# Kernel tuning notes

Measured on AMD Instinct MI355X. Metric: run time of the kernel, lower is better.

Reference implementation:

```python
import jax, jax.numpy as jnp
import numpy as np

DIM = 96
DIM_OUT = 192
HEADS = 2
Q_STRIDE = 4
WINDOW_SIZE = 16  # flattened mask-unit size AFTER q pooling
HEAD_DIM = DIM_OUT // HEADS


def setup_inputs() -> dict:
    key = jax.random.key(0)
    k1, k2, k3, k4, k5 = jax.random.split(key, 5)
    B, N = 64, 3136  # 56x56 tokens, 49 windows of 64 tokens
    x = jax.random.normal(k1, (B, N, DIM), dtype=jnp.float32)
    # nn.Linear params (PyTorch layout: [out, in])
    s_qkv = 1.0 / np.sqrt(DIM)
    w_qkv = jax.random.uniform(k2, (3 * DIM_OUT, DIM), jnp.float32, -s_qkv, s_qkv)
    b_qkv = jax.random.uniform(k3, (3 * DIM_OUT,), jnp.float32, -s_qkv, s_qkv)
    s_proj = 1.0 / np.sqrt(DIM_OUT)
    w_proj = jax.random.uniform(k4, (DIM_OUT, DIM_OUT), jnp.float32, -s_proj, s_proj)
    b_proj = jax.random.uniform(k5, (DIM_OUT,), jnp.float32, -s_proj, s_proj)
    return {"x": x, "w_qkv": w_qkv, "b_qkv": b_qkv, "w_proj": w_proj, "b_proj": b_proj}


def reference(x, w_qkv, b_qkv, w_proj, b_proj):
    B, N, _ = x.shape
    num_windows = N // (Q_STRIDE * WINDOW_SIZE)
    tokens_per_win = Q_STRIDE * WINDOW_SIZE  # 64
    # QKV projection; token axis splits as (tokens_per_win, num_windows)
    qkv = (x @ w_qkv.T + b_qkv).reshape(B, tokens_per_win, num_windows, 3, HEADS, HEAD_DIM)
    qkv = jnp.transpose(qkv, (3, 0, 4, 2, 1, 5))  # [3, B, H, W, T, D]
    q, k, v = qkv[0], qkv[1], qkv[2]
    # q pooling via strided amax over q_stride
    q = q.reshape(B, HEADS, num_windows, Q_STRIDE, WINDOW_SIZE, HEAD_DIM).max(axis=3)
    scale = HEAD_DIM ** (-0.5)
    attn = jax.nn.softmax(jnp.einsum('bhwqd,bhwkd->bhwqk', q * scale, k), axis=-1)
    o = jnp.einsum('bhwqk,bhwkd->bhwqd', attn, v)  # [B, H, W, WINDOW_SIZE, D]
    # transpose(1,3) then flatten -> [B, WINDOW_SIZE*num_windows, dim_out]
    o = jnp.transpose(o, (0, 3, 2, 1, 4)).reshape(B, -1, DIM_OUT)
    return o @ w_proj.T + b_proj
```

## Files before the change

### kernel.cpp

```cpp
#include <hip/hip_runtime.h>


#define NW 49
#define NTOK 3136
#define DIM 96
#define DOUT 192

#define WSQ 0
#define WSBQ 55296
#define WSP 55872
#define WSBP 92736
#define WSTOT 92928

typedef __bf16 bf16x8 __attribute__((ext_vector_type(8)));
typedef float f32x4 __attribute__((ext_vector_type(4)));
typedef unsigned short u16x8 __attribute__((ext_vector_type(8)));
typedef unsigned short u16x4 __attribute__((ext_vector_type(4)));

__device__ __forceinline__ unsigned short f2bf(float f) {
    return __builtin_bit_cast(unsigned short, (__bf16)f);
}
__device__ __forceinline__ float bf2f(unsigned short h) {
    unsigned int u = ((unsigned int)h) << 16;
    return __builtin_bit_cast(float, u);
}

__device__ __forceinline__ bool sniff_fp32(const unsigned short* x16) {
    int sane = 0;
    #pragma unroll
    for (int i = 0; i < 32; ++i) {
        unsigned e = ((unsigned)x16[2 * i] >> 7) & 0xFFu;
        sane += (e >= 100u && e <= 141u) ? 1 : 0;
    }
    return sane < 24;
}

__device__ __forceinline__ bf16x8 ldb(const unsigned short* p) {
    return __builtin_bit_cast(bf16x8, *(const u16x8*)p);
}

__global__ __launch_bounds__(256)
void conv_weights(const void* __restrict__ x,
                  const void* __restrict__ w_qkv, const void* __restrict__ b_qkv,
                  const void* __restrict__ w_proj, const void* __restrict__ b_proj,
                  unsigned short* __restrict__ ws)
{
    const bool f32m = sniff_fp32((const unsigned short*)x);
    int t = blockIdx.x * 256 + threadIdx.x;
    if (t >= WSTOT / 8) return;
    int off = t * 8;
    const void* src;
    int rel;
    if (off < WSBQ)      { src = w_qkv;  rel = off; }
    else if (off < WSP)  { src = b_qkv;  rel = off - WSBQ; }
    else if (off < WSBP) { src = w_proj; rel = off - WSP; }
    else                 { src = b_proj; rel = off - WSBP; }
    u16x8 v;
    if (f32m) {
        const float* p = (const float*)src + rel;
        f32x4 a = *(const f32x4*)p;
        f32x4 bb = *(const f32x4*)(p + 4);
        v[0] = f2bf(a[0]);  v[1] = f2bf(a[1]);  v[2] = f2bf(a[2]);  v[3] = f2bf(a[3]);
        v[4] = f2bf(bb[0]); v[5] = f2bf(bb[1]); v[6] = f2bf(bb[2]); v[7] = f2bf(bb[3]);
    } else {
        v = *(const u16x8*)((const unsigned short*)src + rel);
    }
    *(u16x8*)(ws + off) = v;
}

__global__ __launch_bounds__(256, 2)
void mua_main(const void* __restrict__ x,
              const unsigned short* __restrict__ ws,
              void* __restrict__ out)
{
    const int bid = blockIdx.x;
    const int b   = bid / NW;
    const int wi  = bid - b * NW;
    const int tid  = threadIdx.x;
    const int wave = tid >> 6;
    const int lane = tid & 63;
    const int quad = lane >> 4;
    const int l16  = lane & 15;

    __shared__ __attribute__((aligned(16))) unsigned short lds[19456];
    unsigned short* x_s  = lds;
    unsigned short* k_s  = lds;
    unsigned short* v_s  = lds;
    unsigned short* qp_s = lds + 13824;
    unsigned short* o_s  = lds + 13824;
    unsigned short* p_s  = lds + 17152;

    bf16x8 wq[3][3];
    float  biasq[6];
    #pragma unroll
    for (int nt = 0; nt < 3; ++nt) {
        const int c = (nt * 4 + wave) * 16 + l16;
        #pragma unroll
        for (int ks = 0; ks < 3; ++ks)
            wq[nt][ks] = ldb(ws + WSQ + c * 96 + ks * 32 + quad * 8);
    }
    #pragma unroll
    for (int nt = 0; nt < 6; ++nt)
        biasq[nt] = bf2f(ws[WSBQ + (nt * 4 + wave) * 16 + l16]);

    const bool f32m = sniff_fp32((const unsigned short*)x);

    {
        const size_t xoff = ((size_t)b * NTOK + wi) * DIM;
        if (f32m) {
            #pragma unroll
            for (int i = 0; i < 3; ++i) {
                int chunk = tid + i * 256;
                int row = chunk / 12;
                int c16 = chunk - row * 12;
                const float* p = (const float*)x + xoff + (size_t)row * (NW * DIM) + c16 * 8;
                f32x4 a = *(const f32x4*)p;
                f32x4 bb = *(const f32x4*)(p + 4);
                u16x8 r;
                r[0] = f2bf(a[0]);  r[1] = f2bf(a[1]);  r[2] = f2bf(a[2]);  r[3] = f2bf(a[3]);
                r[4] = f2bf(bb[0]); r[5] = f2bf(bb[1]); r[6] = f2bf(bb[2]); r[7] = f2bf(bb[3]);
                *(u16x8*)&x_s[row * 104 + c16 * 8] = r;
            }
        } else {
            #pragma unroll
            for (int i = 0; i < 3; ++i) {
                int chunk = tid + i * 256;
                int row = chunk / 12;
                int c16 = chunk - row * 12;
                const unsigned short* p = (const unsigned short*)x + xoff + (size_t)row * (NW * DIM) + c16 * 8;
                *(u16x8*)&x_s[row * 104 + c16 * 8] = *(const u16x8*)p;
            }
        }
    }
    __syncthreads();

    bf16x8 afr[4][3];
    #pragma unroll
    for (int mt = 0; mt < 4; ++mt)
        #pragma unroll
        for (int ks = 0; ks < 3; ++ks)
            afr[mt][ks] = ldb(&x_s[(mt * 16 + l16) * 104 + ks * 32 + quad * 8]);
    __syncthreads();

    #pragma unroll
    for (int nt = 0; nt < 6; ++nt) {
        const int slot = nt % 3;
        f32x4 acc[4];
        #pragma unroll
        for (int mt = 0; mt < 4; ++mt) {
            acc[mt] = (f32x4){0.f, 0.f, 0.f, 0.f};
            #pragma unroll
            for (int ks = 0; ks < 3; ++ks)
                acc[mt] = __builtin_amdgcn_mfma_f32_16x16x32_bf16(afr[mt][ks], wq[slot][ks], acc[mt], 0, 0, 0);
        }
        if (nt < 3) {
            const int c2 = ((nt + 3) * 4 + wave) * 16 + l16;
            #pragma unroll
            for (int ks = 0; ks < 3; ++ks)
                wq[slot][ks] = ldb(ws + WSQ + c2 * 96 + ks * 32 + quad * 8);
        }
        const int tt = nt * 4 + wave;
        const float bias = biasq[nt];
        if (nt < 3) {
            const int hd = tt / 6;
            const int d  = (tt % 6) * 16 + l16;
            #pragma unroll
            for (int r = 0; r < 4; ++r) {
                float m = fmaxf(fmaxf(acc[0][r], acc[1][r]), fmaxf(acc[2][r], acc[3][r])) + bias;
                qp_s[(hd * 16 + quad * 4 + r) * 104 + d] = f2bf(m);
            }
        } else {
            const int tk = tt - 12;
            const int hd = tk / 6;
            const int d  = (tk % 6) * 16 + l16;
            #pragma unroll
            for (int mt = 0; mt < 4; ++mt)
                #pragma unroll
                for (int r = 0; r < 4; ++r)
                    k_s[hd * 6656 + (mt * 16 + quad * 4 + r) * 104 + d] = f2bf(acc[mt][r] + bias);
        }
    }
    __syncthreads();

    const int h   = wave >> 1;
    const int sub = wave & 1;
    bf16x8 qa[3];
    #pragma unroll
    for (int ks = 0; ks < 3; ++ks)
        qa[ks] = ldb(&qp_s[(h * 16 + l16) * 104 + ks * 32 + quad * 8]);
    f32x4 s[4];
    #pragma unroll
    for (int nt = 0; nt < 4; ++nt) {
        s[nt] = (f32x4){0.f, 0.f, 0.f, 0.f};
        #pragma unroll
        for (int ks = 0; ks < 3; ++ks) {
            bf16x8 kb = ldb(&k_s[h * 6656 + (nt * 16 + l16) * 104 + ks * 32 + quad * 8]);
            s[nt] = __builtin_amdgcn_mfma_f32_16x16x32_bf16(qa[ks], kb, s[nt], 0, 0, 0);
        }
    }
    float rinv[4];
    const float cexp = 0.10206207261596576f * 1.4426950408889634f;
    #pragma unroll
    for (int r = 0; r < 4; ++r) {
        float m = fmaxf(fmaxf(s[0][r], s[1][r]), fmaxf(s[2][r], s[3][r]));
        m = fmaxf(m, __shfl_xor(m, 1));
        m = fmaxf(m, __shfl_xor(m, 2));
        m = fmaxf(m, __shfl_xor(m, 4));
        m = fmaxf(m, __shfl_xor(m, 8));
        float sum = 0.f;
        #pragma unroll
        for (int nt = 0; nt < 4; ++nt) {
            s[nt][r] = exp2f((s[nt][r] - m) * cexp);
            sum += s[nt][r];
        }
        sum += __shfl_xor(sum, 1);
        sum += __shfl_xor(sum, 2);
        sum += __shfl_xor(sum, 4);
        sum += __shfl_xor(sum, 8);
        rinv[r] = 1.0f / sum;
    }
    if (sub == 0) {
        #pragma unroll
        for (int nt = 0; nt < 4; ++nt)
            #pragma unroll
            for (int r = 0; r < 4; ++r)
                p_s[h * 1152 + (quad * 4 + r) * 72 + nt * 16 + l16] = f2bf(s[nt][r]);
    }

    bf16x8 wv[2][3];
    float  biasv[3];
    #pragma unroll
    for (int i = 0; i < 2; ++i) {
        const int c = 384 + (i * 4 + wave) * 16 + l16;
        #pragma unroll
        for (int ks = 0; ks < 3; ++ks)
            wv[i][ks] = ldb(ws + WSQ + c * 96 + ks * 32 + quad * 8);
    }
    #pragma unroll
    for (int i = 0; i < 3; ++i)
        biasv[i] = bf2f(ws[WSBQ + 384 + (i * 4 + wave) * 16 + l16]);
    __syncthreads();

    #pragma unroll
    for (int i = 0; i < 3; ++i) {
        const int slot = i & 1;
        f32x4 acc[4];
        #pragma unroll
        for (int mt = 0; mt < 4; ++mt) {
            acc[mt] = (f32x4){0.f, 0.f, 0.f, 0.f};
            #pragma unroll
            for (int ks = 0; ks < 3; ++ks)
                acc[mt] = __builtin_amdgcn_mfma_f32_16x16x32_bf16(afr[mt][ks], wv[slot][ks], acc[mt], 0, 0, 0);
        }
        if (i == 0) {
            const int c2 = 384 + (2 * 4 + wave) * 16 + l16;
            #pragma unroll
            for (int ks = 0; ks < 3; ++ks)
                wv[0][ks] = ldb(ws + WSQ + c2 * 96 + ks * 32 + quad * 8);
        }
        const int tv = i * 4 + wave;
        const int hd = tv / 6;
        const int d  = (tv % 6) * 16 + l16;
        const float bias = biasv[i];
        #pragma unroll
        for (int mt = 0; mt < 4; ++mt) {
            u16x4 pk;
            #pragma unroll
            for (int r = 0; r < 4; ++r) pk[r] = f2bf(acc[mt][r] + bias);
            *(u16x4*)&v_s[hd * 6912 + d * 72 + mt * 16 + quad * 4] = pk;
        }
    }

    const int cbase = wave * 48;
    bf16x8 wpr[3][6];
    float  biasp[3];
    #pragma unroll
    for (int i = 0; i < 3; ++i) {
        const int c = cbase + i * 16 + l16;
        #pragma unroll
        for (int ks = 0; ks < 6; ++ks)
            wpr[i][ks] = ldb(ws + WSP + c * 192 + ks * 32 + quad * 8);
        biasp[i] = bf2f(ws[WSBP + c]);
    }
    __syncthreads();

    bf16x8 pa[2];
    #pragma unroll
    for (int ks = 0; ks < 2; ++ks)
        pa[ks] = ldb(&p_s[h * 1152 + l16 * 72 + ks * 32 + quad * 8]);
    #pragma unroll
    for (int i = 0; i < 3; ++i) {
        const int n0 = (sub * 3 + i) * 16;
        f32x4 oacc = (f32x4){0.f, 0.f, 0.f, 0.f};
        #pragma unroll
        for (int ks = 0; ks < 2; ++ks) {
            bf16x8 vb = ldb(&v_s[h * 6912 + (n0 + l16) * 72 + ks * 32 + quad * 8]);
            oacc = __builtin_amdgcn_mfma_f32_16x16x32_bf16(pa[ks], vb, oacc, 0, 0, 0);
        }
        #pragma unroll
        for (int r = 0; r < 4; ++r)
            o_s[(quad * 4 + r) * 200 + h * 96 + n0 + l16] = f2bf(oacc[r] * rinv[r]);
    }
    __syncthreads();

    bf16x8 oa[6];
    #pragma unroll
    for (int ks = 0; ks < 6; ++ks)
        oa[ks] = ldb(&o_s[l16 * 200 + ks * 32 + quad * 8]);
    #pragma unroll
    for (int i = 0; i < 3; ++i) {
        const int c = cbase + i * 16 + l16;
        f32x4 acc = (f32x4){0.f, 0.f, 0.f, 0.f};
        #pragma unroll
        for (int ks = 0; ks < 6; ++ks)
            acc = __builtin_amdgcn_mfma_f32_16x16x32_bf16(oa[ks], wpr[i][ks], acc, 0, 0, 0);
        const float bias = biasp[i];
        #pragma unroll
        for (int r = 0; r < 4; ++r) {
            const int m = quad * 4 + r;
            const size_t idx = ((size_t)(b * 784 + m * NW + wi)) * DOUT + c;
            if (f32m) ((float*)out)[idx] = acc[r] + bias;
            else      ((unsigned short*)out)[idx] = f2bf(acc[r] + bias);
        }
    }
}

extern "C" void kernel_launch(void* const* d_in, const int* in_sizes, int n_in,
                              void* d_out, int out_size, void* d_ws, size_t ws_size,
                              hipStream_t stream) {
    const void* x      = d_in[0];
    const void* w_qkv  = d_in[1];
    const void* b_qkv  = d_in[2];
    const void* w_proj = d_in[3];
    const void* b_proj = d_in[4];
    unsigned short* ws = (unsigned short*)d_ws;

    dim3 gridc((WSTOT / 8 + 255) / 256), blockc(256);
    hipLaunchKernelGGL(conv_weights, gridc, blockc, 0, stream,
                       x, w_qkv, b_qkv, w_proj, b_proj, ws);

    dim3 grid(64 * NW), block(256);
    hipLaunchKernelGGL(mua_main, grid, block, 0, stream, x, ws, d_out);
}
```

Baseline: 176.3 us.

## Compute transposed scores, keep softmax probs in registers, swizzle K/V LDS layouts

The score MFMA now computes S^T (K as the A operand) so each lane holds a full key column. The softmax reduction then uses only cross-quad shuffles. The probabilities are repacked into the PV A-operand with register shuffles instead of going through a p_s LDS buffer. K and V tiles move from padded strides to XOR-swizzled unpadded layouts, which shrinks LDS from 19456 to 15616 shorts and aims to avoid bank conflicts. This removes one LDS round trip and cuts LDS footprint, at the cost of many extra __shfl operations and more complex indexing.

```diff
diff --git a/kernel.cpp b/kernel.cpp
--- a/kernel.cpp
+++ b/kernel.cpp
@@ -16,6 +16,7 @@
 typedef float f32x4 __attribute__((ext_vector_type(4)));
 typedef unsigned short u16x8 __attribute__((ext_vector_type(8)));
 typedef unsigned short u16x4 __attribute__((ext_vector_type(4)));
+typedef unsigned int   u32x4 __attribute__((ext_vector_type(4)));
 
 __device__ __forceinline__ unsigned short f2bf(float f) {
     return __builtin_bit_cast(unsigned short, (__bf16)f);
@@ -82,13 +83,12 @@
     const int quad = lane >> 4;
     const int l16  = lane & 15;
 
-    __shared__ __attribute__((aligned(16))) unsigned short lds[19456];
+    __shared__ __attribute__((aligned(16))) unsigned short lds[15616];
     unsigned short* x_s  = lds;
     unsigned short* k_s  = lds;
     unsigned short* v_s  = lds;
-    unsigned short* qp_s = lds + 13824;
-    unsigned short* o_s  = lds + 13824;
-    unsigned short* p_s  = lds + 17152;
+    unsigned short* qp_s = lds + 12288;
+    unsigned short* o_s  = lds + 12288;
 
     bf16x8 wq[3][3];
     float  biasq[6];
@@ -172,12 +172,14 @@
         } else {
             const int tk = tt - 12;
             const int hd = tk / 6;
-            const int d  = (tk % 6) * 16 + l16;
+            const int dbh  = ((tk % 6) * 16) / 8 + (l16 >> 3);
+            const int dlow = l16 & 7;
             #pragma unroll
             for (int mt = 0; mt < 4; ++mt)
                 #pragma unroll
                 for (int r = 0; r < 4; ++r)
-                    k_s[hd * 6656 + (mt * 16 + quad * 4 + r) * 104 + d] = f2bf(acc[mt][r] + bias);
+                    k_s[hd * 6144 + (mt * 16 + quad * 4 + r) * 96 + ((dbh ^ r) << 3) + dlow]
+                        = f2bf(acc[mt][r] + bias);
         }
     }
     __syncthreads();
@@ -188,43 +190,72 @@
     #pragma unroll
     for (int ks = 0; ks < 3; ++ks)
         qa[ks] = ldb(&qp_s[(h * 16 + l16) * 104 + ks * 32 + quad * 8]);
-    f32x4 s[4];
-    #pragma unroll
-    for (int nt = 0; nt < 4; ++nt) {
-        s[nt] = (f32x4){0.f, 0.f, 0.f, 0.f};
-        #pragma unroll
-        for (int ks = 0; ks < 3; ++ks) {
-            bf16x8 kb = ldb(&k_s[h * 6656 + (nt * 16 + l16) * 104 + ks * 32 + quad * 8]);
-            s[nt] = __builtin_amdgcn_mfma_f32_16x16x32_bf16(qa[ks], kb, s[nt], 0, 0, 0);
-        }
-    }
-    float rinv[4];
+    f32x4 st[4];
+    #pragma unroll
+    for (int mt = 0; mt < 4; ++mt) st[mt] = (f32x4){0.f, 0.f, 0.f, 0.f};
+    #pragma unroll
+    for (int ks = 0; ks < 3; ++ks)
+        #pragma unroll
+        for (int mt = 0; mt < 4; ++mt) {
+            bf16x8 kb = ldb(&k_s[h * 6144 + (mt * 16 + l16) * 96 + (((ks * 4 + quad) ^ (l16 & 3)) << 3)]);
+            st[mt] = __builtin_amdgcn_mfma_f32_16x16x32_bf16(kb, qa[ks], st[mt], 0, 0, 0);
+        }
     const float cexp = 0.10206207261596576f * 1.4426950408889634f;
-    #pragma unroll
-    for (int r = 0; r < 4; ++r) {
-        float m = fmaxf(fmaxf(s[0][r], s[1][r]), fmaxf(s[2][r], s[3][r]));
-        m = fmaxf(m, __shfl_xor(m, 1));
-        m = fmaxf(m, __shfl_xor(m, 2));
-        m = fmaxf(m, __shfl_xor(m, 4));
-        m = fmaxf(m, __shfl_xor(m, 8));
-        float sum = 0.f;
-        #pragma unroll
-        for (int nt = 0; nt < 4; ++nt) {
-            s[nt][r] = exp2f((s[nt][r] - m) * cexp);
-            sum += s[nt][r];
-        }
-        sum += __shfl_xor(sum, 1);
-        sum += __shfl_xor(sum, 2);
-        sum += __shfl_xor(sum, 4);
-        sum += __shfl_xor(sum, 8);
-        rinv[r] = 1.0f / sum;
-    }
-    if (sub == 0) {
-        #pragma unroll
-        for (int nt = 0; nt < 4; ++nt)
-            #pragma unroll
-            for (int r = 0; r < 4; ++r)
-                p_s[h * 1152 + (quad * 4 + r) * 72 + nt * 16 + l16] = f2bf(s[nt][r]);
+    float mx;
+    {
+        float m0 = fmaxf(fmaxf(st[0][0], st[0][1]), fmaxf(st[0][2], st[0][3]));
+        float m1 = fmaxf(fmaxf(st[1][0], st[1][1]), fmaxf(st[1][2], st[1][3]));
+        float m2 = fmaxf(fmaxf(st[2][0], st[2][1]), fmaxf(st[2][2], st[2][3]));
+        float m3 = fmaxf(fmaxf(st[3][0], st[3][1]), fmaxf(st[3][2], st[3][3]));
+        mx = fmaxf(fmaxf(m0, m1), fmaxf(m2, m3));
+    }
+    mx = fmaxf(mx, __shfl_xor(mx, 16));
+    mx = fmaxf(mx, __shfl_xor(mx, 32));
+    float e[4][4];
+    #pragma unroll
+    for (int mt = 0; mt < 4; ++mt)
+        #pragma unroll
+        for (int r = 0; r < 4; ++r)
+            e[mt][r] = exp2f((st[mt][r] - mx) * cexp);
+    float sum;
+    {
+        float s0 = (e[0][0] + e[0][1]) + (e[0][2] + e[0][3]);
+        float s1 = (e[1][0] + e[1][1]) + (e[1][2] + e[1][3]);
+        float s2 = (e[2][0] + e[2][1]) + (e[2][2] + e[2][3]);
+        float s3 = (e[3][0] + e[3][1]) + (e[3][2] + e[3][3]);
+        sum = (s0 + s1) + (s2 + s3);
+    }
+    sum += __shfl_xor(sum, 16);
+    sum += __shfl_xor(sum, 32);
+    const float rinv_l = 1.0f / sum;
+    float rs[4];
+    #pragma unroll
+    for (int r = 0; r < 4; ++r)
+        rs[r] = __shfl(rinv_l, (lane & 48) + quad * 4 + r);
+    unsigned wlo[4], whi[4];
+    #pragma unroll
+    for (int mt = 0; mt < 4; ++mt) {
+        wlo[mt] = (unsigned)f2bf(e[mt][0]) | ((unsigned)f2bf(e[mt][1]) << 16);
+        whi[mt] = (unsigned)f2bf(e[mt][2]) | ((unsigned)f2bf(e[mt][3]) << 16);
+    }
+    bf16x8 pa[2];
+    {
+        const int srcA = ((quad & 1) * 2) * 16 + l16;
+        const int srcB = srcA + 16;
+        const bool hiT = quad >= 2;
+        #pragma unroll
+        for (int ks2 = 0; ks2 < 2; ++ks2) {
+            unsigned lo0a = __shfl(wlo[2 * ks2], srcA), lo0b = __shfl(wlo[2 * ks2 + 1], srcA);
+            unsigned hi0a = __shfl(whi[2 * ks2], srcA), hi0b = __shfl(whi[2 * ks2 + 1], srcA);
+            unsigned lo1a = __shfl(wlo[2 * ks2], srcB), lo1b = __shfl(wlo[2 * ks2 + 1], srcB);
+            unsigned hi1a = __shfl(whi[2 * ks2], srcB), hi1b = __shfl(whi[2 * ks2 + 1], srcB);
+            u32x4 W;
+            W[0] = hiT ? lo0b : lo0a;
+            W[1] = hiT ? hi0b : hi0a;
+            W[2] = hiT ? lo1b : lo1a;
+            W[3] = hiT ? hi1b : hi1a;
+            pa[ks2] = __builtin_bit_cast(bf16x8, W);
+        }
     }
 
     bf16x8 wv[2][3];
@@ -267,7 +298,8 @@
             u16x4 pk;
             #pragma unroll
             for (int r = 0; r < 4; ++r) pk[r] = f2bf(acc[mt][r] + bias);
-            *(u16x4*)&v_s[hd * 6912 + d * 72 + mt * 16 + quad * 4] = pk;
+            const int tb = 2 * mt + (quad >> 1);
+            *(u16x4*)&v_s[hd * 6144 + d * 64 + ((tb ^ (d & 7)) << 3) + (quad & 1) * 4] = pk;
         }
     }
 
@@ -284,22 +316,18 @@
     }
     __syncthreads();
 
-    bf16x8 pa[2];
-    #pragma unroll
-    for (int ks = 0; ks < 2; ++ks)
-        pa[ks] = ldb(&p_s[h * 1152 + l16 * 72 + ks * 32 + quad * 8]);
     #pragma unroll
     for (int i = 0; i < 3; ++i) {
         const int n0 = (sub * 3 + i) * 16;
         f32x4 oacc = (f32x4){0.f, 0.f, 0.f, 0.f};
         #pragma unroll
-        for (int ks = 0; ks < 2; ++ks) {
-            bf16x8 vb = ldb(&v_s[h * 6912 + (n0 + l16) * 72 + ks * 32 + quad * 8]);
-            oacc = __builtin_amdgcn_mfma_f32_16x16x32_bf16(pa[ks], vb, oacc, 0, 0, 0);
+        for (int ks2 = 0; ks2 < 2; ++ks2) {
+            bf16x8 vb = ldb(&v_s[h * 6144 + (n0 + l16) * 64 + (((ks2 * 4 + quad) ^ (l16 & 7)) << 3)]);
+            oacc = __builtin_amdgcn_mfma_f32_16x16x32_bf16(pa[ks2], vb, oacc, 0, 0, 0);
         }
         #pragma unroll
         for (int r = 0; r < 4; ++r)
-            o_s[(quad * 4 + r) * 200 + h * 96 + n0 + l16] = f2bf(oacc[r] * rinv[r]);
+            o_s[(quad * 4 + r) * 200 + h * 96 + n0 + l16] = f2bf(oacc[r] * rs[r]);
     }
     __syncthreads();
 
```

Result: no change. 179.4 us (+1.8%).
